# Kernel tuning notes

Measured on AMD Instinct MI355X. Metric: run time of the kernel, lower is better.

## Reference

```python
import jax, jax.numpy as jnp
import numpy as np
from jax import lax

HIDDEN = 64
INPUT = 16
SEQ = 2048
BATCH = 2048


def setup_inputs() -> dict:
    key = jax.random.key(0)
    k1, k2, k3, k4, k5 = jax.random.split(key, 5)
    # scale weights down so tanh recurrence stays in a sane dynamic range
    return {
        "x": jax.random.normal(k1, (SEQ, BATCH, INPUT), dtype=jnp.float32),
        "w_weight": 0.1 * jax.random.normal(k2, (HIDDEN, HIDDEN), dtype=jnp.float32),
        "w_bias": 0.1 * jax.random.normal(k3, (HIDDEN,), dtype=jnp.float32),
        "v_weight": 0.1 * jax.random.normal(k4, (HIDDEN, INPUT), dtype=jnp.float32),
        "v_bias": 0.1 * jax.random.normal(k5, (HIDDEN,), dtype=jnp.float32),
    }


def reference(x, w_weight, w_bias, v_weight, v_bias):
    # x: [S, B, I]. Precompute the input projection for all timesteps at once
    # (one big GEMM instead of S tiny ones): vx[s] = x[s] @ v_weight.T + v_bias
    vx = jnp.einsum('sbi,hi->sbh', x, v_weight) + v_bias  # [S, B, H]

    h0 = jnp.zeros((x.shape[1], w_weight.shape[0]), dtype=x.dtype)  # [B, H]

    def step(h, vx_t):
        # h_new = tanh(W h + b_w + V x_t + b_v); self.b in the original is
        # a constant zeros vector and contributes nothing.
        h_new = jnp.tanh(h @ w_weight.T + w_bias + vx_t)
        return h_new, h_new

    _, h_seq = lax.scan(step, h0, vx)  # h_seq: [S, B, H]
    h = h_seq[-1]                       # [B, H] (matches torch code, not docstring)
    return h_seq, h
```

## Files before the change

### kernel.cpp

```cpp
#include <hip/hip_runtime.h>


typedef short short8v __attribute__((ext_vector_type(8)));
typedef float f32x4   __attribute__((ext_vector_type(4)));

constexpr int S = 2048, B = 2048, I = 16, H = 64;
constexpr int RB = 16;
constexpr int XR = 24;
constexpr int NT = 448;

static __device__ __forceinline__ unsigned short f2bf(float f) {
    unsigned u = __builtin_bit_cast(unsigned, f);
    return (unsigned short)((u + 0x7FFFu + ((u >> 16) & 1u)) >> 16);
}
static __device__ __forceinline__ unsigned cvtpk(float lo, float hi) {
    unsigned r;
    asm("v_cvt_pk_bf16_f32 %0, %1, %2" : "=v"(r) : "v"(lo), "v"(hi));
    return r;
}
static __device__ __forceinline__ float tanh_fast(float p) {
    float e = __builtin_amdgcn_exp2f(p * 2.8853900817779268f);
    return fmaf(-2.0f, __builtin_amdgcn_rcpf(e + 1.0f), 1.0f);
}
static __device__ __forceinline__ float bflo(unsigned d) {
    return __builtin_bit_cast(float, d << 16);
}
static __device__ __forceinline__ float bfhi(unsigned d) {
    return __builtin_bit_cast(float, d & 0xFFFF0000u);
}

#define MFMA(A, Bf, C) __builtin_amdgcn_mfma_f32_16x16x32_bf16((A), (Bf), (C), 0, 0, 0)
#define LDS_BARRIER()                                         \
    do {                                                      \
        asm volatile("s_waitcnt lgkmcnt(0)" ::: "memory");    \
        __builtin_amdgcn_s_barrier();                         \
        asm volatile("" ::: "memory");                        \
    } while (0)

__global__ __launch_bounds__(NT)
__attribute__((amdgpu_waves_per_eu(1, 2)))
void rnn_split4(const float* __restrict__ x,
                const float* __restrict__ Wm,
                const float* __restrict__ wb,
                const float* __restrict__ Vm,
                const float* __restrict__ vb,
                float* __restrict__ out)
{
    const int tid = threadIdx.x;
    const int wv  = tid >> 6;
    const int l   = tid & 63;
    const int c   = l & 15;
    const int g   = l >> 4;
    const int b0  = blockIdx.x * RB;

    __shared__ __align__(16) unsigned short xs[2][8][RB][XR];
    __shared__ __align__(8)  uint2 exch[2][4][64];

    for (int q = tid; q < 2 * 8 * RB * XR / 2; q += NT)
        ((unsigned*)&xs[0][0][0][0])[q] = 0u;
    for (int q = tid; q < 2 * 4 * 64 * 2; q += NT)
        ((unsigned*)&exch[0][0][0])[q] = 0u;
    for (int q = tid; q < 512; q += NT) {
        int i4 = q & 3, cc = (q >> 2) & 15, tc = q >> 6;
        float4 t4 = *(const float4*)(x + ((size_t)tc * B + b0 + cc) * I + 4 * i4);
        uint2 p;
        p.x = cvtpk(t4.x, t4.y);
        p.y = cvtpk(t4.z, t4.w);
        *(uint2*)(&xs[0][tc][cc][4 * i4]) = p;
    }
    __syncthreads();

    if (wv < 4) {
        const int m = wv;
        short8v Wlo, Whi, VA;
        f32x4 bs;
        {
            const int o = 32 * (m >> 1) + 8 * (c >> 2) + 4 * (m & 1) + (c & 3);
            const float* wr = Wm + o * H + 8 * g;
#pragma unroll
            for (int j = 0; j < 8; ++j) {
                Wlo[j] = (short)f2bf(wr[j]);
                Whi[j] = (short)f2bf(wr[32 + j]);
            }
            const float* vr = Vm + o * I;
#pragma unroll
            for (int j = 0; j < 8; ++j) {
                int k = 8 * g + j;
                VA[j] = (k < I) ? (short)f2bf(vr[k]) : (short)0;
            }
            const int ob = 32 * (m >> 1) + 8 * g + 4 * (m & 1);
            bs[0] = wb[ob] + vb[ob];
            bs[1] = wb[ob + 1] + vb[ob + 1];
            bs[2] = wb[ob + 2] + vb[ob + 2];
            bs[3] = wb[ob + 3] + vb[ob + 3];
        }
        const int xi = (g < 2) ? 8 * g : 16;

        for (int chunk = 0; chunk < S / 8; ++chunk) {
            const unsigned short* xb = &xs[chunk & 1][0][c][xi];
            short8v BX0 = *(const short8v*)(xb + 0 * RB * XR);
            short8v BX1 = *(const short8v*)(xb + 1 * RB * XR);
            short8v BX2 = *(const short8v*)(xb + 2 * RB * XR);
            short8v BX3 = *(const short8v*)(xb + 3 * RB * XR);
            short8v BX4 = *(const short8v*)(xb + 4 * RB * XR);
            short8v BX5 = *(const short8v*)(xb + 5 * RB * XR);
            short8v BX6 = *(const short8v*)(xb + 6 * RB * XR);
            short8v BX7 = *(const short8v*)(xb + 7 * RB * XR);

#define STEP(tq, BXs)                                                         \
            {                                                                 \
                const int t = chunk * 8 + (tq);                               \
                uint2 q0 = exch[t & 1][0][l];                                 \
                uint2 q1 = exch[t & 1][1][l];                                 \
                uint2 q2 = exch[t & 1][2][l];                                 \
                uint2 q3 = exch[t & 1][3][l];                                 \
                uint4 b0v; b0v.x = q0.x; b0v.y = q0.y; b0v.z = q1.x; b0v.w = q1.y; \
                uint4 b1v; b1v.x = q2.x; b1v.y = q2.y; b1v.z = q3.x; b1v.w = q3.y; \
                short8v B0h = __builtin_bit_cast(short8v, b0v);               \
                short8v B1h = __builtin_bit_cast(short8v, b1v);               \
                f32x4 a = bs;                                                 \
                a = MFMA(VA, BXs, a);       \
                a = MFMA(Wlo, B0h, a);                                        \
                a = MFMA(Whi, B1h, a);                                        \
                float h0 = tanh_fast(a[0]), h1 = tanh_fast(a[1]);             \
                float h2 = tanh_fast(a[2]), h3 = tanh_fast(a[3]);             \
                uint2 nb;                                                     \
                nb.x = cvtpk(h0, h1);                                         \
                nb.y = cvtpk(h2, h3);                                         \
                exch[(t + 1) & 1][m][l] = nb;                                 \
                LDS_BARRIER();                                                \
            }
            STEP(0, BX0) STEP(1, BX1) STEP(2, BX2) STEP(3, BX3)
            STEP(4, BX4) STEP(5, BX5) STEP(6, BX6) STEP(7, BX7)
#undef STEP
        }
    } else if (wv < 6) {
        const int cw   = wv - 4;
        const int offq = 32 * cw;
        for (int t = 0; t < S; ++t) {
            if (t >= 1) {
                uint2 ra = exch[t & 1][2 * cw][l];
                uint2 rb = exch[t & 1][2 * cw + 1][l];
                float4 ha, hb;
                ha.x = bflo(ra.x); ha.y = bfhi(ra.x);
                ha.z = bflo(ra.y); ha.w = bfhi(ra.y);
                hb.x = bflo(rb.x); hb.y = bfhi(rb.x);
                hb.z = bflo(rb.y); hb.w = bfhi(rb.y);
                float* op = out + ((size_t)(t - 1) * B + b0 + c) * H + 8 * g + offq;
                *(float4*)(op + 0) = ha;
                *(float4*)(op + 4) = hb;
            }
            LDS_BARRIER();
        }
        {
            uint2 ra = exch[0][2 * cw][l];
            uint2 rb = exch[0][2 * cw + 1][l];
            float4 ha, hb;
            ha.x = bflo(ra.x); ha.y = bfhi(ra.x);
            ha.z = bflo(ra.y); ha.w = bfhi(ra.y);
            hb.x = bflo(rb.x); hb.y = bfhi(rb.x);
            hb.z = bflo(rb.y); hb.w = bfhi(rb.y);
            float* op = out + ((size_t)(S - 1) * B + b0 + c) * H + 8 * g + offq;
            *(float4*)(op + 0) = ha;
            *(float4*)(op + 4) = hb;
            float* fp = out + (size_t)S * B * H + (size_t)(b0 + c) * H + 8 * g + offq;
            *(float4*)(fp + 0) = ha;
            *(float4*)(fp + 4) = hb;
        }
    } else {
        float4 ld0, ld1, ld2, ld3, ld4, ld5, ld6, ld7;
        for (int t = 0; t < S; ++t) {
            const int k = t >> 3;
            if ((t & 7) == 0 && k + 1 < S / 8) {
                const float* xb = x + (size_t)(k + 1) * 8 * B * I;
#define LD(m2, dst)                                                        \
                {                                                          \
                    int q = l + 64 * (m2);                                 \
                    int i4 = q & 3, cc = (q >> 2) & 15, tc = q >> 6;       \
                    dst = *(const float4*)(xb + ((size_t)tc * B + b0 + cc) * I + 4 * i4); \
                }
                LD(0, ld0) LD(1, ld1) LD(2, ld2) LD(3, ld3)
                LD(4, ld4) LD(5, ld5) LD(6, ld6) LD(7, ld7)
#undef LD
            }
            if ((t & 7) == 4 && k + 1 < S / 8) {
                asm volatile("s_waitcnt vmcnt(0)" ::: "memory");
                const int buf = (k + 1) & 1;
#define WR(m2, src)                                                        \
                {                                                          \
                    int q = l + 64 * (m2);                                 \
                    int i4 = q & 3, cc = (q >> 2) & 15, tc = q >> 6;       \
                    uint2 p;                                               \
                    p.x = cvtpk(src.x, src.y);                             \
                    p.y = cvtpk(src.z, src.w);                             \
                    *(uint2*)(&xs[buf][tc][cc][4 * i4]) = p;               \
                }
                WR(0, ld0) WR(1, ld1) WR(2, ld2) WR(3, ld3)
                WR(4, ld4) WR(5, ld5) WR(6, ld6) WR(7, ld7)
#undef WR
            }
            LDS_BARRIER();
        }
    }
}

extern "C" void kernel_launch(void* const* d_in, const int* in_sizes, int n_in,
                              void* d_out, int out_size, void* d_ws, size_t ws_size,
                              hipStream_t stream) {
    const float* x  = (const float*)d_in[0];
    const float* Wm = (const float*)d_in[1];
    const float* wb = (const float*)d_in[2];
    const float* Vm = (const float*)d_in[3];
    const float* vb = (const float*)d_in[4];
    float* out = (float*)d_out;

    rnn_split4<<<B / RB, NT, 0, stream>>>(x, Wm, wb, Vm, vb, out);
}
```

Baseline: 464.0 us.

## Process two 16-row batch tiles per block to interleave independent MFMA chains

```diff
diff --git a/kernel.cpp b/kernel.cpp
--- a/kernel.cpp
+++ b/kernel.cpp
@@ -38,35 +38,35 @@
     } while (0)
 
 __global__ __launch_bounds__(NT)
-__attribute__((amdgpu_waves_per_eu(1, 2)))
-void rnn_split4(const float* __restrict__ x,
-                const float* __restrict__ Wm,
-                const float* __restrict__ wb,
-                const float* __restrict__ Vm,
-                const float* __restrict__ vb,
-                float* __restrict__ out)
+__attribute__((amdgpu_waves_per_eu(1)))
+void rnn_2tile(const float* __restrict__ x,
+               const float* __restrict__ Wm,
+               const float* __restrict__ wb,
+               const float* __restrict__ Vm,
+               const float* __restrict__ vb,
+               float* __restrict__ out)
 {
     const int tid = threadIdx.x;
     const int wv  = tid >> 6;
     const int l   = tid & 63;
     const int c   = l & 15;
     const int g   = l >> 4;
-    const int b0  = blockIdx.x * RB;
-
-    __shared__ __align__(16) unsigned short xs[2][8][RB][XR];
-    __shared__ __align__(8)  uint2 exch[2][4][64];
-
-    for (int q = tid; q < 2 * 8 * RB * XR / 2; q += NT)
-        ((unsigned*)&xs[0][0][0][0])[q] = 0u;
-    for (int q = tid; q < 2 * 4 * 64 * 2; q += NT)
-        ((unsigned*)&exch[0][0][0])[q] = 0u;
-    for (int q = tid; q < 512; q += NT) {
-        int i4 = q & 3, cc = (q >> 2) & 15, tc = q >> 6;
-        float4 t4 = *(const float4*)(x + ((size_t)tc * B + b0 + cc) * I + 4 * i4);
+    const int bB  = blockIdx.x * 2 * RB;
+
+    __shared__ __align__(16) unsigned short xs[2][8][2][RB][XR];
+    __shared__ __align__(8)  uint2 exch[2][2][4][64];
+
+    for (int q = tid; q < (int)(sizeof(xs) / 4); q += NT)
+        ((unsigned*)&xs[0][0][0][0][0])[q] = 0u;
+    for (int q = tid; q < (int)(sizeof(exch) / 4); q += NT)
+        ((unsigned*)&exch[0][0][0][0])[q] = 0u;
+    for (int q = tid; q < 1024; q += NT) {
+        int i4 = q & 3, cc = (q >> 2) & 15, tl = (q >> 6) & 1, tc = q >> 7;
+        float4 t4 = *(const float4*)(x + ((size_t)tc * B + bB + tl * RB + cc) * I + 4 * i4);
         uint2 p;
         p.x = cvtpk(t4.x, t4.y);
         p.y = cvtpk(t4.z, t4.w);
-        *(uint2*)(&xs[0][tc][cc][4 * i4]) = p;
+        *(uint2*)(&xs[0][tc][tl][cc][4 * i4]) = p;
     }
     __syncthreads();
 
@@ -97,78 +97,101 @@
         const int xi = (g < 2) ? 8 * g : 16;
 
         for (int chunk = 0; chunk < S / 8; ++chunk) {
-            const unsigned short* xb = &xs[chunk & 1][0][c][xi];
-            short8v BX0 = *(const short8v*)(xb + 0 * RB * XR);
-            short8v BX1 = *(const short8v*)(xb + 1 * RB * XR);
-            short8v BX2 = *(const short8v*)(xb + 2 * RB * XR);
-            short8v BX3 = *(const short8v*)(xb + 3 * RB * XR);
-            short8v BX4 = *(const short8v*)(xb + 4 * RB * XR);
-            short8v BX5 = *(const short8v*)(xb + 5 * RB * XR);
-            short8v BX6 = *(const short8v*)(xb + 6 * RB * XR);
-            short8v BX7 = *(const short8v*)(xb + 7 * RB * XR);
-
-#define STEP(tq, BXs)                                                         \
-            {                                                                 \
-                const int t = chunk * 8 + (tq);                               \
-                uint2 q0 = exch[t & 1][0][l];                                 \
-                uint2 q1 = exch[t & 1][1][l];                                 \
-                uint2 q2 = exch[t & 1][2][l];                                 \
-                uint2 q3 = exch[t & 1][3][l];                                 \
-                uint4 b0v; b0v.x = q0.x; b0v.y = q0.y; b0v.z = q1.x; b0v.w = q1.y; \
-                uint4 b1v; b1v.x = q2.x; b1v.y = q2.y; b1v.z = q3.x; b1v.w = q3.y; \
-                short8v B0h = __builtin_bit_cast(short8v, b0v);               \
-                short8v B1h = __builtin_bit_cast(short8v, b1v);               \
-                f32x4 a = bs;                                                 \
-                a = MFMA(VA, BXs, a);       \
-                a = MFMA(Wlo, B0h, a);                                        \
-                a = MFMA(Whi, B1h, a);                                        \
-                float h0 = tanh_fast(a[0]), h1 = tanh_fast(a[1]);             \
-                float h2 = tanh_fast(a[2]), h3 = tanh_fast(a[3]);             \
-                uint2 nb;                                                     \
-                nb.x = cvtpk(h0, h1);                                         \
-                nb.y = cvtpk(h2, h3);                                         \
-                exch[(t + 1) & 1][m][l] = nb;                                 \
-                LDS_BARRIER();                                                \
-            }
-            STEP(0, BX0) STEP(1, BX1) STEP(2, BX2) STEP(3, BX3)
-            STEP(4, BX4) STEP(5, BX5) STEP(6, BX6) STEP(7, BX7)
+#pragma unroll
+            for (int half = 0; half < 2; ++half) {
+                const unsigned short* xb =
+                    &xs[chunk & 1][half * 4][0][c][xi];
+                const int SSTEP = 2 * RB * XR;
+                short8v BXa0 = *(const short8v*)(xb + 0 * SSTEP);
+                short8v BXb0 = *(const short8v*)(xb + 0 * SSTEP + RB * XR);
+                short8v BXa1 = *(const short8v*)(xb + 1 * SSTEP);
+                short8v BXb1 = *(const short8v*)(xb + 1 * SSTEP + RB * XR);
+                short8v BXa2 = *(const short8v*)(xb + 2 * SSTEP);
+                short8v BXb2 = *(const short8v*)(xb + 2 * SSTEP + RB * XR);
+                short8v BXa3 = *(const short8v*)(xb + 3 * SSTEP);
+                short8v BXb3 = *(const short8v*)(xb + 3 * SSTEP + RB * XR);
+
+#define STEP(tq, BXa, BXb)                                                    \
+                {                                                             \
+                    const int t = chunk * 8 + half * 4 + (tq);                \
+                    uint2 qa0 = exch[t & 1][0][0][l];                         \
+                    uint2 qa1 = exch[t & 1][0][1][l];                         \
+                    uint2 qa2 = exch[t & 1][0][2][l];                         \
+                    uint2 qa3 = exch[t & 1][0][3][l];                         \
+                    uint2 qb0 = exch[t & 1][1][0][l];                         \
+                    uint2 qb1 = exch[t & 1][1][1][l];                         \
+                    uint2 qb2 = exch[t & 1][1][2][l];                         \
+                    uint2 qb3 = exch[t & 1][1][3][l];                         \
+                    uint4 v0a; v0a.x = qa0.x; v0a.y = qa0.y; v0a.z = qa1.x; v0a.w = qa1.y; \
+                    uint4 v1a; v1a.x = qa2.x; v1a.y = qa2.y; v1a.z = qa3.x; v1a.w = qa3.y; \
+                    uint4 v0b; v0b.x = qb0.x; v0b.y = qb0.y; v0b.z = qb1.x; v0b.w = qb1.y; \
+                    uint4 v1b; v1b.x = qb2.x; v1b.y = qb2.y; v1b.z = qb3.x; v1b.w = qb3.y; \
+                    short8v B0a = __builtin_bit_cast(short8v, v0a);           \
+                    short8v B1a = __builtin_bit_cast(short8v, v1a);           \
+                    short8v B0b = __builtin_bit_cast(short8v, v0b);           \
+                    short8v B1b = __builtin_bit_cast(short8v, v1b);           \
+                    f32x4 aa = bs, ab = bs;                                   \
+                    aa = MFMA(VA, BXa, aa);  ab = MFMA(VA, BXb, ab);          \
+                    aa = MFMA(Wlo, B0a, aa); ab = MFMA(Wlo, B0b, ab);         \
+                    aa = MFMA(Whi, B1a, aa); ab = MFMA(Whi, B1b, ab);         \
+                    float ha0 = tanh_fast(aa[0]), ha1 = tanh_fast(aa[1]);     \
+                    float ha2 = tanh_fast(aa[2]), ha3 = tanh_fast(aa[3]);     \
+                    float hb0 = tanh_fast(ab[0]), hb1 = tanh_fast(ab[1]);     \
+                    float hb2 = tanh_fast(ab[2]), hb3 = tanh_fast(ab[3]);     \
+                    uint2 na, nb;                                             \
+                    na.x = cvtpk(ha0, ha1); na.y = cvtpk(ha2, ha3);           \
+                    nb.x = cvtpk(hb0, hb1); nb.y = cvtpk(hb2, hb3);           \
+                    exch[(t + 1) & 1][0][m][l] = na;                          \
+                    exch[(t + 1) & 1][1][m][l] = nb;                          \
+                    LDS_BARRIER();                                            \
+                }
+                STEP(0, BXa0, BXb0)
+                STEP(1, BXa1, BXb1)
+                STEP(2, BXa2, BXb2)
+                STEP(3, BXa3, BXb3)
 #undef STEP
+            }
         }
     } else if (wv < 6) {
         const int cw   = wv - 4;
         const int offq = 32 * cw;
         for (int t = 0; t < S; ++t) {
             if (t >= 1) {
-                uint2 ra = exch[t & 1][2 * cw][l];
-                uint2 rb = exch[t & 1][2 * cw + 1][l];
-                float4 ha, hb;
-                ha.x = bflo(ra.x); ha.y = bfhi(ra.x);
-                ha.z = bflo(ra.y); ha.w = bfhi(ra.y);
-                hb.x = bflo(rb.x); hb.y = bfhi(rb.x);
-                hb.z = bflo(rb.y); hb.w = bfhi(rb.y);
-                float* op = out + ((size_t)(t - 1) * B + b0 + c) * H + 8 * g + offq;
-                *(float4*)(op + 0) = ha;
-                *(float4*)(op + 4) = hb;
+#pragma unroll
+                for (int tl = 0; tl < 2; ++tl) {
+                    uint2 ra = exch[t & 1][tl][2 * cw][l];
+                    uint2 rb = exch[t & 1][tl][2 * cw + 1][l];
+                    float4 ha, hb;
+                    ha.x = bflo(ra.x); ha.y = bfhi(ra.x);
+                    ha.z = bflo(ra.y); ha.w = bfhi(ra.y);
+                    hb.x = bflo(rb.x); hb.y = bfhi(rb.x);
+                    hb.z = bflo(rb.y); hb.w = bfhi(rb.y);
+                    float* op = out + ((size_t)(t - 1) * B + bB + tl * RB + c) * H + 8 * g + offq;
+                    *(float4*)(op + 0) = ha;
+                    *(float4*)(op + 4) = hb;
+                }
             }
             LDS_BARRIER();
         }
-        {
-            uint2 ra = exch[0][2 * cw][l];
-            uint2 rb = exch[0][2 * cw + 1][l];
+#pragma unroll
+        for (int tl = 0; tl < 2; ++tl) {
+            uint2 ra = exch[0][tl][2 * cw][l];
+            uint2 rb = exch[0][tl][2 * cw + 1][l];
             float4 ha, hb;
             ha.x = bflo(ra.x); ha.y = bfhi(ra.x);
             ha.z = bflo(ra.y); ha.w = bfhi(ra.y);
             hb.x = bflo(rb.x); hb.y = bfhi(rb.x);
             hb.z = bflo(rb.y); hb.w = bfhi(rb.y);
-            float* op = out + ((size_t)(S - 1) * B + b0 + c) * H + 8 * g + offq;
+            float* op = out + ((size_t)(S - 1) * B + bB + tl * RB + c) * H + 8 * g + offq;
             *(float4*)(op + 0) = ha;
             *(float4*)(op + 4) = hb;
-            float* fp = out + (size_t)S * B * H + (size_t)(b0 + c) * H + 8 * g + offq;
+            float* fp = out + (size_t)S * B * H + (size_t)(bB + tl * RB + c) * H + 8 * g + offq;
             *(float4*)(fp + 0) = ha;
             *(float4*)(fp + 4) = hb;
         }
     } else {
-        float4 ld0, ld1, ld2, ld3, ld4, ld5, ld6, ld7;
+        float4 d00, d01, d02, d03, d04, d05, d06, d07;
+        float4 d08, d09, d10, d11, d12, d13, d14, d15;
         for (int t = 0; t < S; ++t) {
             const int k = t >> 3;
             if ((t & 7) == 0 && k + 1 < S / 8) {
@@ -176,11 +199,14 @@
 #define LD(m2, dst)                                                        \
                 {                                                          \
                     int q = l + 64 * (m2);                                 \
-                    int i4 = q & 3, cc = (q >> 2) & 15, tc = q >> 6;       \
-                    dst = *(const float4*)(xb + ((size_t)tc * B + b0 + cc) * I + 4 * i4); \
-                }
-                LD(0, ld0) LD(1, ld1) LD(2, ld2) LD(3, ld3)
-                LD(4, ld4) LD(5, ld5) LD(6, ld6) LD(7, ld7)
+                    int i4 = q & 3, cc = (q >> 2) & 15;                    \
+                    int tl = (q >> 6) & 1, tc = q >> 7;                    \
+                    dst = *(const float4*)(xb + ((size_t)tc * B + bB + tl * RB + cc) * I + 4 * i4); \
+                }
+                LD(0, d00)  LD(1, d01)  LD(2, d02)  LD(3, d03)
+                LD(4, d04)  LD(5, d05)  LD(6, d06)  LD(7, d07)
+                LD(8, d08)  LD(9, d09)  LD(10, d10) LD(11, d11)
+                LD(12, d12) LD(13, d13) LD(14, d14) LD(15, d15)
 #undef LD
             }
             if ((t & 7) == 4 && k + 1 < S / 8) {
@@ -189,14 +215,17 @@
 #define WR(m2, src)                                                        \
                 {                                                          \
                     int q = l + 64 * (m2);                                 \
-                    int i4 = q & 3, cc = (q >> 2) & 15, tc = q >> 6;       \
+                    int i4 = q & 3, cc = (q >> 2) & 15;                    \
+                    int tl = (q >> 6) & 1, tc = q >> 7;                    \
                     uint2 p;                                               \
                     p.x = cvtpk(src.x, src.y);                             \
                     p.y = cvtpk(src.z, src.w);                             \
-                    *(uint2*)(&xs[buf][tc][cc][4 * i4]) = p;               \
-                }
-                WR(0, ld0) WR(1, ld1) WR(2, ld2) WR(3, ld3)
-                WR(4, ld4) WR(5, ld5) WR(6, ld6) WR(7, ld7)
+                    *(uint2*)(&xs[buf][tc][tl][cc][4 * i4]) = p;           \
+                }
+                WR(0, d00)  WR(1, d01)  WR(2, d02)  WR(3, d03)
+                WR(4, d04)  WR(5, d05)  WR(6, d06)  WR(7, d07)
+                WR(8, d08)  WR(9, d09)  WR(10, d10) WR(11, d11)
+                WR(12, d12) WR(13, d13) WR(14, d14) WR(15, d15)
 #undef WR
             }
             LDS_BARRIER();
@@ -214,5 +243,5 @@
     const float* vb = (const float*)d_in[4];
     float* out = (float*)d_out;
 
-    rnn_split4<<<B / RB, NT, 0, stream>>>(x, Wm, wb, Vm, vb, out);
-}
+    rnn_2tile<<<B / (2 * RB), NT, 0, stream>>>(x, Wm, wb, Vm, vb, out);
+}
```

After: 737.3 us. +58.9%, slower.
